# Optimization experiments

Measured on AMD Instinct MI355X. Metric: run time of the kernel, lower is better.

The kernel has to match this reference:

```python
import jax, jax.numpy as jnp
import numpy as np

EPS = 1e-5

def _bn(x):
    # training-mode batchnorm (batch stats), gamma=1 beta=0 per the module's init
    ax = tuple(range(x.ndim - 1))
    m = x.mean(ax, keepdims=True)
    v = x.var(ax, keepdims=True)
    return (x - m) * jax.lax.rsqrt(v + EPS)

def _mlp(x, weights):
    # shared 1x1-conv MLP: pointwise linear -> BN -> ReLU
    for W in weights:
        x = jax.nn.relu(_bn(jnp.einsum('...c,oc->...o', x, W)))
    return x

def _fps_single(xyz, npoint):
    # farthest point sampling, xyz [N,3] -> [npoint] int32 indices
    N = xyz.shape[0]
    def step(carry, _):
        dists, far = carry
        d = jnp.sum((xyz - xyz[far]) ** 2, -1)
        dists = jnp.minimum(dists, d)
        return (dists, jnp.argmax(dists).astype(jnp.int32)), far
    init = (jnp.full((N,), 1e10, xyz.dtype), jnp.int32(0))
    _, idx = jax.lax.scan(step, init, None, length=npoint)
    return idx

def _ball_query(new_xyz, xyz, radius, nsample):
    # first nsample points (in original order) within radius of each center
    d2 = jnp.sum((new_xyz[:, :, None, :] - xyz[:, None, :, :]) ** 2, -1)  # [B,S,N]
    N = xyz.shape[1]
    rank = jnp.where(d2 < radius * radius, jnp.arange(N, dtype=jnp.int32), jnp.int32(N))
    vals, _ = jax.lax.top_k(-rank, nsample)
    idx = -vals
    idx = jnp.where(idx == N, idx[..., :1], idx)  # pad with first valid (center itself)
    return idx

def _gather(pts, idx):
    # pts [B,N,C], idx [B,S,ns] -> [B,S,ns,C]
    B, S, ns = idx.shape
    return jnp.take_along_axis(pts, idx.reshape(B, S * ns, 1), axis=1).reshape(B, S, ns, pts.shape[-1])

def _sa(xyz, feats, npoint, radius, nsample, weights):
    fps_idx = jax.vmap(_fps_single, in_axes=(0, None))(xyz, npoint)
    new_xyz = jnp.take_along_axis(xyz, fps_idx[:, :, None], axis=1)  # [B,S,3]
    idx = _ball_query(new_xyz, xyz, radius, nsample)
    g_xyz = (_gather(xyz, idx) - new_xyz[:, :, None, :]) / radius  # normalize_xyz
    x = g_xyz if feats is None else jnp.concatenate([g_xyz, _gather(feats, idx)], -1)
    x = _mlp(x, weights)
    return new_xyz, x.max(axis=2), fps_idx  # maxpool over nsample

def _forward(obj_cloud, gripper_cloud, sa1_w0, sa1_w1, sa1_w2, sa2_w0, sa2_w1, sa2_w2,
             sa3_w0, sa3_w1, sa3_w2, ge_w0, ge_w1, ge_w2,
             head_w0, head_b0, head_w1, head_b1, head_w2, head_b2):
    # gripper encoder: pointwise conv1d MLP + global maxpool
    g = _mlp(gripper_cloud, [ge_w0, ge_w1, ge_w2])      # [B,G,128]
    gripper_feature = g.max(axis=1)                      # [B,128]
    # backbone
    xyz1, f1, _ = _sa(obj_cloud, None, 512, 0.2, 32, [sa1_w0, sa1_w1, sa1_w2])
    xyz2, f2, _ = _sa(xyz1, f1, 128, 0.4, 64, [sa2_w0, sa2_w1, sa2_w2])
    # sa3: group_all (use_xyz, no centering/normalization)
    x = jnp.concatenate([xyz2, f2], -1)[:, None]         # [B,1,128,259]
    x = _mlp(x, [sa3_w0, sa3_w1, sa3_w2])
    obj_feature = x.max(axis=2)[:, 0]                    # [B,1024]
    comb = jnp.concatenate([gripper_feature, obj_feature], -1)  # [B,1152]
    h = _bn(comb)
    h = jax.nn.relu(_bn(h @ head_w0.T + head_b0))
    h = jax.nn.relu(_bn(h @ head_w1.T + head_b1))
    return jax.nn.relu(h @ head_w2.T + head_b2)          # [B,1]

def setup_inputs() -> dict:
    key = jax.random.key(0)
    ks = jax.random.split(key, 24)
    def w(k, o, i):
        return (jax.random.normal(k, (o, i), jnp.float32) * 0.05)
    inp = {
        'obj_cloud': jax.random.uniform(ks[0], (8, 20000, 3), jnp.float32),
        'gripper_cloud': jax.random.uniform(ks[1], (8, 512, 3), jnp.float32),
        'sa1_w0': w(ks[2], 64, 3),   'sa1_w1': w(ks[3], 64, 64),   'sa1_w2': w(ks[4], 128, 64),
        'sa2_w0': w(ks[5], 128, 131),'sa2_w1': w(ks[6], 128, 128), 'sa2_w2': w(ks[7], 256, 128),
        'sa3_w0': w(ks[8], 256, 259),'sa3_w1': w(ks[9], 512, 256), 'sa3_w2': w(ks[10], 1024, 512),
        'ge_w0': w(ks[11], 64, 3),   'ge_w1': w(ks[12], 128, 64),  'ge_w2': w(ks[13], 128, 128),
        'head_w0': w(ks[14], 512, 1152), 'head_b0': jnp.zeros((512,), jnp.float32),
        'head_w1': w(ks[15], 256, 512),  'head_b1': jnp.zeros((256,), jnp.float32),
        'head_w2': w(ks[16], 1, 256),    'head_b2': jnp.zeros((1,), jnp.float32),
    }
    return inp

def reference(obj_cloud, gripper_cloud, sa1_w0, sa1_w1, sa1_w2, sa2_w0, sa2_w1, sa2_w2,
              sa3_w0, sa3_w1, sa3_w2, ge_w0, ge_w1, ge_w2,
              head_w0, head_b0, head_w1, head_b1, head_w2, head_b2):
    return _forward(obj_cloud, gripper_cloud, sa1_w0, sa1_w1, sa1_w2, sa2_w0, sa2_w1, sa2_w2,
                    sa3_w0, sa3_w1, sa3_w2, ge_w0, ge_w1, ge_w2,
                    head_w0, head_b0, head_w1, head_b1, head_w2, head_b2)
```

## Files before the change

### kernel.cpp

```cpp
#include <hip/hip_runtime.h>
#include <cstddef>
#include <cstdint>

#define EPS_BN 1e-5f
#define NBINS 4
#define NEG_INF (-__builtin_inff())

template <bool FUSE_IN, bool FUSE_MAX>
__global__ __launch_bounds__(256) void gemm_xwt(const float* __restrict__ X,
                                                const float* __restrict__ Wm,
                                                float* __restrict__ Y,
                                                int R, int Cin, int Cout,
                                                const float* __restrict__ st_in, int Rin,
                                                float* __restrict__ st_out,
                                                float* __restrict__ pooled, int ns) {
  __shared__ __align__(16) float Xs[16][132];
  __shared__ __align__(16) float Ws[16][132];
  __shared__ float sMean[512], sScale[512];
  const int t  = threadIdx.x;
  const int r0 = blockIdx.x << 7;
  const int n0 = blockIdx.y << 7;
  const int tx = t & 15;
  const int ty = t >> 4;

  if constexpr (FUSE_IN) {
    const float inv = 1.f / (float)Rin;
    for (int k = t; k < Cin; k += 256) {
      float s = 0.f, q = 0.f;
#pragma unroll
      for (int bn = 0; bn < NBINS; ++bn) {
        s += st_in[bn * 2 * Cin + k];
        q += st_in[bn * 2 * Cin + Cin + k];
      }
      const float m  = s * inv;
      const float vr = fmaf(-m, m, q * inv);
      sMean[k]  = m;
      sScale[k] = rsqrtf(vr + EPS_BN);
    }
    __syncthreads();
  }

  float acc[8][8] = {};
  const int rStage = t >> 1;
  const int kBase  = (t & 1) << 3;
  const int nr     = n0 + rStage;

  for (int k0 = 0; k0 < Cin; k0 += 16) {
    const float* xrow = X  + (size_t)(r0 + rStage) * Cin + k0 + kBase;
    const float* wrow = Wm + (size_t)nr * Cin + k0 + kBase;
    if (((Cin & 3) == 0) && (k0 + 16 <= Cin)) {
      float4 xa = *(const float4*)(xrow);
      float4 xb = *(const float4*)(xrow + 4);
      if constexpr (FUSE_IN) {
        const int kb = k0 + kBase;
        xa.x = fmaxf(0.f, (xa.x - sMean[kb + 0]) * sScale[kb + 0]);
        xa.y = fmaxf(0.f, (xa.y - sMean[kb + 1]) * sScale[kb + 1]);
        xa.z = fmaxf(0.f, (xa.z - sMean[kb + 2]) * sScale[kb + 2]);
        xa.w = fmaxf(0.f, (xa.w - sMean[kb + 3]) * sScale[kb + 3]);
        xb.x = fmaxf(0.f, (xb.x - sMean[kb + 4]) * sScale[kb + 4]);
        xb.y = fmaxf(0.f, (xb.y - sMean[kb + 5]) * sScale[kb + 5]);
        xb.z = fmaxf(0.f, (xb.z - sMean[kb + 6]) * sScale[kb + 6]);
        xb.w = fmaxf(0.f, (xb.w - sMean[kb + 7]) * sScale[kb + 7]);
      }
      Xs[kBase + 0][rStage] = xa.x; Xs[kBase + 1][rStage] = xa.y;
      Xs[kBase + 2][rStage] = xa.z; Xs[kBase + 3][rStage] = xa.w;
      Xs[kBase + 4][rStage] = xb.x; Xs[kBase + 5][rStage] = xb.y;
      Xs[kBase + 6][rStage] = xb.z; Xs[kBase + 7][rStage] = xb.w;
      float4 wa = {0, 0, 0, 0}, wb = {0, 0, 0, 0};
      if (nr < Cout) { wa = *(const float4*)(wrow); wb = *(const float4*)(wrow + 4); }
      Ws[kBase + 0][rStage] = wa.x; Ws[kBase + 1][rStage] = wa.y;
      Ws[kBase + 2][rStage] = wa.z; Ws[kBase + 3][rStage] = wa.w;
      Ws[kBase + 4][rStage] = wb.x; Ws[kBase + 5][rStage] = wb.y;
      Ws[kBase + 6][rStage] = wb.z; Ws[kBase + 7][rStage] = wb.w;
    } else {
#pragma unroll
      for (int u = 0; u < 8; ++u) {
        const int k = k0 + kBase + u;
        float xe = 0.f, we = 0.f;
        if (k < Cin) {
          xe = xrow[u];
          if constexpr (FUSE_IN) xe = fmaxf(0.f, (xe - sMean[k]) * sScale[k]);
          if (nr < Cout) we = wrow[u];
        }
        Xs[kBase + u][rStage] = xe;
        Ws[kBase + u][rStage] = we;
      }
    }
    __syncthreads();
#pragma unroll
    for (int kk = 0; kk < 16; ++kk) {
      const float4 a0 = *(const float4*)(&Xs[kk][ty << 2]);
      const float4 a1 = *(const float4*)(&Xs[kk][64 + (ty << 2)]);
      const float4 b0 = *(const float4*)(&Ws[kk][tx << 2]);
      const float4 b1 = *(const float4*)(&Ws[kk][64 + (tx << 2)]);
      const float av[8] = {a0.x, a0.y, a0.z, a0.w, a1.x, a1.y, a1.z, a1.w};
      const float bw[8] = {b0.x, b0.y, b0.z, b0.w, b1.x, b1.y, b1.z, b1.w};
#pragma unroll
      for (int i = 0; i < 8; ++i)
#pragma unroll
        for (int j = 0; j < 8; ++j) acc[i][j] = fmaf(av[i], bw[j], acc[i][j]);
    }
    __syncthreads();
  }
  if constexpr (!FUSE_MAX) {
#pragma unroll
    for (int h = 0; h < 2; ++h)
#pragma unroll
      for (int i = 0; i < 4; ++i) {
        const int r = r0 + h * 64 + (ty << 2) + i;
        float* yr = Y + (size_t)r * Cout;
#pragma unroll
        for (int g = 0; g < 2; ++g) {
          const int n = n0 + g * 64 + (tx << 2);
          if (n < Cout) {
            float4 o = {acc[h * 4 + i][g * 4 + 0], acc[h * 4 + i][g * 4 + 1],
                        acc[h * 4 + i][g * 4 + 2], acc[h * 4 + i][g * 4 + 3]};
            *(float4*)(yr + n) = o;
          }
        }
      }
  }
#pragma unroll
  for (int g = 0; g < 2; ++g)
#pragma unroll
    for (int j = 0; j < 4; ++j) {
      float s = 0.f, q = 0.f;
#pragma unroll
      for (int rh = 0; rh < 8; ++rh) {
        const float v = acc[rh][g * 4 + j];
        s += v;
        q = fmaf(v, v, q);
      }
      Xs[ty][g * 64 + (tx << 2) + j] = s;
      Ws[ty][g * 64 + (tx << 2) + j] = q;
    }
  __syncthreads();
  if (t < 128) {
    const int n = n0 + t;
    if (n < Cout) {
      float s = 0.f, q = 0.f;
#pragma unroll
      for (int w = 0; w < 16; ++w) { s += Xs[w][t]; q += Ws[w][t]; }
      float* dst = st_out + (blockIdx.x & (NBINS - 1)) * 2 * Cout;
      atomicAdd(dst + n, s);
      atomicAdd(dst + Cout + n, q);
    }
  }
  if constexpr (FUSE_MAX) {
    __syncthreads();
    float mxAll = NEG_INF;
#pragma unroll
    for (int h = 0; h < 2; ++h) {
#pragma unroll
      for (int g2 = 0; g2 < 2; ++g2)
#pragma unroll
        for (int j = 0; j < 4; ++j) {
          float mx = acc[h * 4 + 0][g2 * 4 + j];
          mx = fmaxf(mx, acc[h * 4 + 1][g2 * 4 + j]);
          mx = fmaxf(mx, acc[h * 4 + 2][g2 * 4 + j]);
          mx = fmaxf(mx, acc[h * 4 + 3][g2 * 4 + j]);
          Xs[ty][g2 * 64 + (tx << 2) + j] = mx;
        }
      __syncthreads();
      if (t < 128) {
        const int n = n0 + t;
        if (n < Cout) {
          if (ns <= 64) {
            const int tpg = ns >> 2;
            const int gph = 64 / ns;
            for (int gq = 0; gq < gph; ++gq) {
              float mx = NEG_INF;
              for (int w = gq * tpg; w < gq * tpg + tpg; ++w) mx = fmaxf(mx, Xs[w][t]);
              const int g = (r0 + h * 64) / ns + gq;
              pooled[(size_t)g * Cout + n] = mx;
            }
          } else {
            float mx = NEG_INF;
            for (int w = 0; w < 16; ++w) mx = fmaxf(mx, Xs[w][t]);
            mxAll = fmaxf(mxAll, mx);
          }
        }
      }
      __syncthreads();
    }
    if (ns > 64 && t < 128) {
      const int n = n0 + t;
      if (n < Cout) pooled[(size_t)(r0 >> 7) * Cout + n] = mxAll;
    }
  }
}

__global__ void bn_apply_pooled(const float* __restrict__ P, const float* __restrict__ st,
                                float* __restrict__ o, int G, int C, int Rtrue) {
  const int i = blockIdx.x * 256 + threadIdx.x;
  if (i >= G * C) return;
  const int c = i % C;
  float s = 0.f, q = 0.f;
#pragma unroll
  for (int bn = 0; bn < NBINS; ++bn) {
    s += st[bn * 2 * C + c];
    q += st[bn * 2 * C + C + c];
  }
  const float inv = 1.f / (float)Rtrue;
  const float m  = s * inv;
  const float vr = fmaf(-m, m, q * inv);
  const float sc = rsqrtf(vr + EPS_BN);
  o[i] = fmaxf(0.f, (P[i] - m) * sc);
}

__global__ void bn_apply_relu_maxpool(const float* __restrict__ Y,
                                      const float* __restrict__ st,
                                      float* __restrict__ o, int G, int ns, int C) {
  const int i = blockIdx.x * 256 + threadIdx.x;
  if (i >= G * C) return;
  const int c = i % C;
  const int g = i / C;
  float s = 0.f, q = 0.f;
#pragma unroll
  for (int bn = 0; bn < NBINS; ++bn) {
    s += st[bn * 2 * C + c];
    q += st[bn * 2 * C + C + c];
  }
  const int R = G * ns;
  const float inv = 1.f / (float)R;
  const float m  = s * inv;
  const float vr = fmaf(-m, m, q * inv);
  const float sc = rsqrtf(vr + EPS_BN);
  const float* p = Y + (size_t)g * ns * C + c;
  float mx = NEG_INF;
  for (int k = 0; k < ns; ++k) mx = fmaxf(mx, p[(size_t)k * C]);
  o[i] = fmaxf(0.f, (mx - m) * sc);
}

#define REPA(X) X(0) X(1) X(2) X(3) X(4) X(5) X(6) X(7) X(8) X(9) X(10) X(11)
#define REPB(X) X(12) X(13) X(14) X(15) X(16) X(17) X(18) X(19)

__global__ __launch_bounds__(1024)
void fps_sa1_kernel(const float* __restrict__ xyz, float* __restrict__ new_xyz) {
  const int b    = blockIdx.x;
  const int tid  = threadIdx.x;
  const int lane = tid & 63;
  const int wave = tid >> 6;
  const float* p = xyz + (size_t)b * 20000 * 3;

  __shared__ float ddL[12 * 1024];
  __shared__ float sv[16], sx[16], sy[16], sz[16];
  __shared__ int   si[16];
  __shared__ float bc[3];

#define DECLR(k) float px##k, py##k, pz##k, dd##k;
  REPB(DECLR)
#undef DECLR

#define INITL(k) ddL[(k) * 1024 + tid] = 1e10f;
  REPA(INITL)
#undef INITL
#define INITR(k) {                                                          \
    const int i = tid + (k) * 1024;                                         \
    if (i < 20000) {                                                        \
      px##k = p[i * 3 + 0]; py##k = p[i * 3 + 1]; pz##k = p[i * 3 + 2];     \
      dd##k = 1e10f;                                                        \
    } else {                                                                \
      px##k = 0.f; py##k = 0.f; pz##k = 0.f;                                \
      dd##k = NEG_INF;                                                      \
    } }
  REPB(INITR)
#undef INITR

  float fx = p[0], fy = p[1], fz = p[2];
  if (tid == 0) {
    float* o = new_xyz + (size_t)b * 512 * 3;
    o[0] = fx; o[1] = fy; o[2] = fz;
  }
  __syncthreads();

  for (int s = 1; s < 512; ++s) {
    float bv = NEG_INF;
    int   bi = 0x7fffffff;
    float bx = 0.f, by = 0.f, bz = 0.f;
#define SCANS(k) {                                                          \
    const int i = tid + (k) * 1024;                                         \
    const float qx = p[i * 3 + 0], qy = p[i * 3 + 1], qz = p[i * 3 + 2];    \
    const float dx = qx - fx, dy = qy - fy, dz = qz - fz;                   \
    const float d  = __fadd_rn(__fadd_rn(__fmul_rn(dx, dx), __fmul_rn(dy, dy)), \
                               __fmul_rn(dz, dz));                          \
    const float nd = fminf(ddL[(k) * 1024 + tid], d);                       \
    ddL[(k) * 1024 + tid] = nd;                                             \
    if (nd > bv) { bv = nd; bi = i; bx = qx; by = qy; bz = qz; } }
    REPA(SCANS)
#undef SCANS
#define SCANR(k) {                                                          \
    const float dx = px##k - fx, dy = py##k - fy, dz = pz##k - fz;          \
    const float d  = __fadd_rn(__fadd_rn(__fmul_rn(dx, dx), __fmul_rn(dy, dy)), \
                               __fmul_rn(dz, dz));                          \
    const float nd = fminf(dd##k, d);                                       \
    dd##k = nd;                                                             \
    if (nd > bv) { bv = nd; bi = tid + (k) * 1024;                          \
                   bx = px##k; by = py##k; bz = pz##k; } }
    REPB(SCANR)
#undef SCANR
    float v  = bv;
    int   i0 = bi;
#pragma unroll
    for (int m = 1; m < 64; m <<= 1) {
      const float ov = __shfl_xor(v, m, 64);
      const int   oi = __shfl_xor(i0, m, 64);
      if (ov > v || (ov == v && oi < i0)) { v = ov; i0 = oi; }
    }
    if (i0 == bi) {
      sv[wave] = bv; si[wave] = bi; sx[wave] = bx; sy[wave] = by; sz[wave] = bz;
    }
    __syncthreads();
    if (tid < 64) {
      const float lv = (lane < 16) ? sv[lane] : NEG_INF;
      const int   li = (lane < 16) ? si[lane] : 0x7fffffff;
      float v2 = lv;
      int   i2 = li;
#pragma unroll
      for (int m = 1; m < 16; m <<= 1) {
        const float ov = __shfl_xor(v2, m, 64);
        const int   oi = __shfl_xor(i2, m, 64);
        if (ov > v2 || (ov == v2 && oi < i2)) { v2 = ov; i2 = oi; }
      }
      if (lane < 16 && li == i2) {
        const float wx = sx[lane], wy = sy[lane], wz = sz[lane];
        bc[0] = wx; bc[1] = wy; bc[2] = wz;
        float* o = new_xyz + ((size_t)b * 512 + s) * 3;
        o[0] = wx; o[1] = wy; o[2] = wz;
      }
    }
    __syncthreads();
    fx = bc[0]; fy = bc[1]; fz = bc[2];
  }
}

template <int N, int NP, int THREADS, int NPT>
__global__ __launch_bounds__(THREADS)
void fps2_kernel(const float* __restrict__ xyz, float* __restrict__ new_xyz) {
  constexpr int NW = THREADS / 64;
  const int b    = blockIdx.x;
  const int tid  = threadIdx.x;
  const int lane = tid & 63;
  const int wave = tid >> 6;
  const float* p = xyz + (size_t)b * N * 3;
  float px[NPT], py[NPT], pz[NPT], dd[NPT];
#pragma unroll
  for (int j = 0; j < NPT; ++j) {
    const int i = tid + j * THREADS;
    if (i < N) {
      px[j] = p[i * 3 + 0];
      py[j] = p[i * 3 + 1];
      pz[j] = p[i * 3 + 2];
      dd[j] = 1e10f;
    } else {
      px[j] = 0.f; py[j] = 0.f; pz[j] = 0.f;
      dd[j] = NEG_INF;
    }
  }
  __shared__ float sv[NW], sx[NW], sy[NW], sz[NW];
  __shared__ int   si[NW];
  __shared__ float bc[3];
  float fx = p[0], fy = p[1], fz = p[2];
  if (tid == 0) {
    float* o = new_xyz + (size_t)b * NP * 3;
    o[0] = fx; o[1] = fy; o[2] = fz;
  }
  for (int s = 1; s < NP; ++s) {
    float bv = NEG_INF;
    int   bi = 0x7fffffff;
    float bx = 0.f, by = 0.f, bz = 0.f;
#pragma unroll
    for (int j = 0; j < NPT; ++j) {
      const float dx = px[j] - fx;
      const float dy = py[j] - fy;
      const float dz = pz[j] - fz;
      const float d  = __fadd_rn(__fadd_rn(__fmul_rn(dx, dx), __fmul_rn(dy, dy)),
                                 __fmul_rn(dz, dz));
      const float nd = fminf(dd[j], d);
      dd[j] = nd;
      if (nd > bv) { bv = nd; bi = tid + j * THREADS; bx = px[j]; by = py[j]; bz = pz[j]; }
    }
    float v = bv;
    int   i0 = bi;
#pragma unroll
    for (int m = 1; m < 64; m <<= 1) {
      const float ov = __shfl_xor(v, m, 64);
      const int   oi = __shfl_xor(i0, m, 64);
      if (ov > v || (ov == v && oi < i0)) { v = ov; i0 = oi; }
    }
    if (i0 == bi) {
      sv[wave] = bv; si[wave] = bi; sx[wave] = bx; sy[wave] = by; sz[wave] = bz;
    }
    __syncthreads();
    if (tid < 64) {
      const float lv = (lane < NW) ? sv[lane] : NEG_INF;
      const int   li = (lane < NW) ? si[lane] : 0x7fffffff;
      float v2 = lv;
      int   i2 = li;
#pragma unroll
      for (int m = 1; m < NW; m <<= 1) {
        const float ov = __shfl_xor(v2, m, 64);
        const int   oi = __shfl_xor(i2, m, 64);
        if (ov > v2 || (ov == v2 && oi < i2)) { v2 = ov; i2 = oi; }
      }
      if (lane < NW && li == i2) {
        const float wx = sx[lane], wy = sy[lane], wz = sz[lane];
        bc[0] = wx; bc[1] = wy; bc[2] = wz;
        float* o = new_xyz + ((size_t)b * NP + s) * 3;
        o[0] = wx; o[1] = wy; o[2] = wz;
      }
    }
    __syncthreads();
    fx = bc[0]; fy = bc[1]; fz = bc[2];
  }
}

template <int N, int NS>
__global__ __launch_bounds__(256)
void ballquery_wave_kernel(const float* __restrict__ centers,
                           const float* __restrict__ pts,
                           int* __restrict__ idx, int BS, int S, float r2) {
  const int w    = (blockIdx.x * 256 + threadIdx.x) >> 6;
  const int lane = threadIdx.x & 63;
  if (w >= BS) return;
  const int b = w / S;
  const float cx = centers[w * 3 + 0];
  const float cy = centers[w * 3 + 1];
  const float cz = centers[w * 3 + 2];
  const float* p = pts + (size_t)b * N * 3;
  int* o = idx + (size_t)w * NS;
  int total = 0;
  int first = -1;
  for (int i0 = 0; i0 < N && total < NS; i0 += 64) {
    const int i = i0 + lane;
    bool pred = false;
    if (i < N) {
      const float dx = cx - p[i * 3 + 0];
      const float dy = cy - p[i * 3 + 1];
      const float dz = cz - p[i * 3 + 2];
      const float d2 = __fadd_rn(__fadd_rn(__fmul_rn(dx, dx), __fmul_rn(dy, dy)),
                                 __fmul_rn(dz, dz));
      pred = (d2 < r2);
    }
    const unsigned long long mask = __ballot(pred);
    if (mask) {
      const unsigned long long below = (lane == 0) ? 0ull : (mask << (64 - lane));
      const int before = __popcll(below);
      if (pred && (total + before) < NS) o[total + before] = i;
      if (first < 0) first = i0 + (__ffsll((long long)mask) - 1);
      total += __popcll(mask);
    }
  }
  if (lane >= total && lane < NS) o[lane] = first;
}

__global__ void group1_kernel(const float* __restrict__ xyz, const float* __restrict__ ctr,
                              const int* __restrict__ idx, float* __restrict__ X1) {
  const int t = blockIdx.x * 256 + threadIdx.x;
  if (t >= 8 * 512 * 32) return;
  const int g = t >> 5;
  const int b = g >> 9;
  const int i = idx[t];
  const float* p = xyz + ((size_t)b * 20000 + i) * 3;
  const float* c = ctr + (size_t)g * 3;
  X1[t * 3 + 0] = (p[0] - c[0]) / 0.2f;
  X1[t * 3 + 1] = (p[1] - c[1]) / 0.2f;
  X1[t * 3 + 2] = (p[2] - c[2]) / 0.2f;
}

__global__ void group2_kernel(const float* __restrict__ xyz1,
                              const float* __restrict__ xyz2,
                              const float* __restrict__ f1,
                              const int* __restrict__ idx2,
                              float* __restrict__ X2) {
  const int t = blockIdx.x * 256 + threadIdx.x;
  if (t >= 65536 * 131) return;
  const int r = t / 131;
  const int c = t - r * 131;
  const int g = r >> 6;
  const int b = g >> 7;
  const int i = idx2[r];
  float v;
  if (c < 3) {
    v = (xyz1[((size_t)b * 512 + i) * 3 + c] - xyz2[(size_t)g * 3 + c]) / 0.4f;
  } else {
    v = f1[((size_t)b * 512 + i) * 128 + (c - 3)];
  }
  X2[t] = v;
}

__global__ void build_x3_kernel(const float* __restrict__ xyz2, const float* __restrict__ f2,
                                float* __restrict__ X3) {
  const int t = blockIdx.x * 256 + threadIdx.x;
  if (t >= 1024 * 259) return;
  const int r = t / 259;
  const int c = t - r * 259;
  X3[t] = (c < 3) ? xyz2[r * 3 + c] : f2[(size_t)r * 256 + (c - 3)];
}

__global__ __launch_bounds__(512) void head_kernel(
    const float* __restrict__ gfeat, const float* __restrict__ objf,
    const float* __restrict__ w0, const float* __restrict__ b0,
    const float* __restrict__ w1, const float* __restrict__ b1,
    const float* __restrict__ w2, const float* __restrict__ b2,
    float* __restrict__ out) {
  __shared__ __align__(16) float comb[8 * 1152];
  __shared__ __align__(16) float h1[8 * 512];
  __shared__ __align__(16) float h2[8 * 256];
  const int tid = threadIdx.x;
  for (int i = tid; i < 8 * 1152; i += 512) {
    const int b = i / 1152, c = i - b * 1152;
    comb[i] = (c < 128) ? gfeat[b * 128 + c] : objf[b * 1024 + (c - 128)];
  }
  __syncthreads();
  for (int c = tid; c < 1152; c += 512) {
    float s = 0.f;
#pragma unroll
    for (int b = 0; b < 8; ++b) s += comb[b * 1152 + c];
    const float m = s * 0.125f;
    float v = 0.f;
#pragma unroll
    for (int b = 0; b < 8; ++b) { const float d = comb[b * 1152 + c] - m; v = fmaf(d, d, v); }
    const float sc = rsqrtf(v * 0.125f + EPS_BN);
#pragma unroll
    for (int b = 0; b < 8; ++b) comb[b * 1152 + c] = (comb[b * 1152 + c] - m) * sc;
  }
  __syncthreads();
  {
    float a[8];
#pragma unroll
    for (int b = 0; b < 8; ++b) a[b] = b0[tid];
    const float* wr = w0 + (size_t)tid * 1152;
    for (int ci = 0; ci < 1152; ci += 4) {
      const float4 wv = *(const float4*)(wr + ci);
#pragma unroll
      for (int b = 0; b < 8; ++b) {
        const float4 xv = *(const float4*)(&comb[b * 1152 + ci]);
        a[b] = fmaf(xv.x, wv.x, a[b]);
        a[b] = fmaf(xv.y, wv.y, a[b]);
        a[b] = fmaf(xv.z, wv.z, a[b]);
        a[b] = fmaf(xv.w, wv.w, a[b]);
      }
    }
    float s = 0.f;
#pragma unroll
    for (int b = 0; b < 8; ++b) s += a[b];
    const float m = s * 0.125f;
    float v = 0.f;
#pragma unroll
    for (int b = 0; b < 8; ++b) { const float d = a[b] - m; v = fmaf(d, d, v); }
    const float sc = rsqrtf(v * 0.125f + EPS_BN);
#pragma unroll
    for (int b = 0; b < 8; ++b) h1[b * 512 + tid] = fmaxf(0.f, (a[b] - m) * sc);
  }
  __syncthreads();
  if (tid < 256) {
    float a[8];
#pragma unroll
    for (int b = 0; b < 8; ++b) a[b] = b1[tid];
    const float* wr = w1 + (size_t)tid * 512;
    for (int ci = 0; ci < 512; ci += 4) {
      const float4 wv = *(const float4*)(wr + ci);
#pragma unroll
      for (int b = 0; b < 8; ++b) {
        const float4 xv = *(const float4*)(&h1[b * 512 + ci]);
        a[b] = fmaf(xv.x, wv.x, a[b]);
        a[b] = fmaf(xv.y, wv.y, a[b]);
        a[b] = fmaf(xv.z, wv.z, a[b]);
        a[b] = fmaf(xv.w, wv.w, a[b]);
      }
    }
    float s = 0.f;
#pragma unroll
    for (int b = 0; b < 8; ++b) s += a[b];
    const float m = s * 0.125f;
    float v = 0.f;
#pragma unroll
    for (int b = 0; b < 8; ++b) { const float d = a[b] - m; v = fmaf(d, d, v); }
    const float sc = rsqrtf(v * 0.125f + EPS_BN);
#pragma unroll
    for (int b = 0; b < 8; ++b) h2[b * 256 + tid] = fmaxf(0.f, (a[b] - m) * sc);
  }
  __syncthreads();
  if (tid < 8) {
    float s = b2[0];
    for (int ci = 0; ci < 256; ++ci) s = fmaf(h2[tid * 256 + ci], w2[ci], s);
    out[tid] = fmaxf(0.f, s);
  }
}

extern "C" void kernel_launch(void* const* d_in, const int* in_sizes, int n_in,
                              void* d_out, int out_size, void* d_ws, size_t ws_size,
                              hipStream_t stream) {
  (void)in_sizes; (void)n_in; (void)out_size; (void)ws_size;
  const float* obj  = (const float*)d_in[0];
  const float* grip = (const float*)d_in[1];
  const float* s1w0 = (const float*)d_in[2];
  const float* s1w1 = (const float*)d_in[3];
  const float* s1w2 = (const float*)d_in[4];
  const float* s2w0 = (const float*)d_in[5];
  const float* s2w1 = (const float*)d_in[6];
  const float* s2w2 = (const float*)d_in[7];
  const float* s3w0 = (const float*)d_in[8];
  const float* s3w1 = (const float*)d_in[9];
  const float* s3w2 = (const float*)d_in[10];
  const float* gw0  = (const float*)d_in[11];
  const float* gw1  = (const float*)d_in[12];
  const float* gw2  = (const float*)d_in[13];
  const float* hw0  = (const float*)d_in[14];
  const float* hb0  = (const float*)d_in[15];
  const float* hw1  = (const float*)d_in[16];
  const float* hb1  = (const float*)d_in[17];
  const float* hw2  = (const float*)d_in[18];
  const float* hb2  = (const float*)d_in[19];
  float* out = (float*)d_out;

  float* wsf   = (float*)d_ws;
  float* stats = wsf;
  float* xyz1  = wsf + 23040;
  float* xyz2  = wsf + 35328;
  float* gfeat = wsf + 38400;
  float* objf  = wsf + 39424;
  float* f1    = wsf + 47616;
  float* f2    = wsf + 571904;
  float* x3    = wsf + 834048;
  int*   idx1  = (int*)(wsf + 1099264);
  int*   idx2  = (int*)(wsf + 1230336);
  float* bufP  = wsf + 1295872;
  float* bufQ  = wsf + 18073088;

  static const int st_off[12] = {0, 512, 1536, 2560, 3072, 3584,
                                 4608, 5632, 6656, 8704, 10752, 14848};
  auto st = [&](int li) { return stats + st_off[li]; };

  hipMemsetAsync(stats, 0, 23040 * sizeof(float), stream);

  auto gemm0 = [&](const float* X, const float* Wm, float* Y, int R, int Cin, int Cout,
                   int lo) {
    dim3 g((R + 127) / 128, (Cout + 127) / 128);
    gemm_xwt<false, false><<<g, 256, 0, stream>>>(X, Wm, Y, R, Cin, Cout, nullptr, 0,
                                                  st(lo), nullptr, 0);
  };
  auto gemmf = [&](const float* X, const float* Wm, float* Y, int R, int Cin, int Cout,
                   int li, int lo) {
    dim3 g((R + 127) / 128, (Cout + 127) / 128);
    gemm_xwt<true, false><<<g, 256, 0, stream>>>(X, Wm, Y, R, Cin, Cout, st(li), R,
                                                 st(lo), nullptr, 0);
  };
  auto gemmfM = [&](const float* X, const float* Wm, float* pooled, int R, int Cin,
                    int Cout, int li, int lo, int ns) {
    dim3 g((R + 127) / 128, (Cout + 127) / 128);
    gemm_xwt<true, true><<<g, 256, 0, stream>>>(X, Wm, nullptr, R, Cin, Cout, st(li), R,
                                                st(lo), pooled, ns);
  };
  auto applymax_k = [&](const float* Y, int li, int G, int ns, int C, float* o) {
    const int n = G * C;
    bn_apply_relu_maxpool<<<(n + 255) / 256, 256, 0, stream>>>(Y, st(li), o, G, ns, C);
  };
  auto applypool_k = [&](const float* P, int li, int G, int C, int Rtrue, float* o) {
    const int n = G * C;
    bn_apply_pooled<<<(n + 255) / 256, 256, 0, stream>>>(P, st(li), o, G, C, Rtrue);
  };

  fps_sa1_kernel<<<8, 1024, 0, stream>>>(obj, xyz1);

  float* gY1 = bufP;
  float* gY2 = bufP + 262144;
  float* gY3 = bufP + 786432;
  gemm0(grip, gw0, gY1, 4096, 3, 64, 0);
  gemmf(gY1, gw1, gY2, 4096, 64, 128, 0, 1);
  gemmf(gY2, gw2, gY3, 4096, 128, 128, 1, 2);
  applymax_k(gY3, 2, 8, 512, 128, gfeat);

  ballquery_wave_kernel<20000, 32><<<1024, 256, 0, stream>>>(xyz1, obj, idx1, 4096, 512, 0.04f);
  float* X1 = bufQ;
  group1_kernel<<<512, 256, 0, stream>>>(obj, xyz1, idx1, X1);
  gemm0(X1, s1w0, bufP, 131072, 3, 64, 3);
  gemmf(bufP, s1w1, bufQ, 131072, 64, 64, 3, 4);
  gemmfM(bufQ, s1w2, bufP, 131072, 64, 128, 4, 5, 32);
  applypool_k(bufP, 5, 4096, 128, 131072, f1);

  fps2_kernel<512, 128, 256, 2><<<8, 256, 0, stream>>>(xyz1, xyz2);
  ballquery_wave_kernel<512, 64><<<256, 256, 0, stream>>>(xyz2, xyz1, idx2, 1024, 128, 0.16f);
  float* X2 = bufQ;
  group2_kernel<<<(65536 * 131 + 255) / 256, 256, 0, stream>>>(xyz1, xyz2, f1, idx2, X2);
  gemm0(X2, s2w0, bufP, 65536, 131, 128, 6);
  gemmf(bufP, s2w1, bufQ, 65536, 128, 128, 6, 7);
  gemmfM(bufQ, s2w2, bufP, 65536, 128, 256, 7, 8, 64);
  applypool_k(bufP, 8, 1024, 256, 65536, f2);

  build_x3_kernel<<<(1024 * 259 + 255) / 256, 256, 0, stream>>>(xyz2, f2, x3);
  float* Y3a = bufQ;
  float* Y3b = bufQ + 262144;
  float* Y3p = bufQ + 786432;
  gemm0(x3, s3w0, Y3a, 1024, 259, 256, 9);
  gemmf(Y3a, s3w1, Y3b, 1024, 256, 512, 9, 10);
  gemmfM(Y3b, s3w2, Y3p, 1024, 512, 1024, 10, 11, 128);
  applypool_k(Y3p, 11, 8, 1024, 1024, objf);

  head_kernel<<<1, 512, 0, stream>>>(gfeat, objf, hw0, hb0, hw1, hb1, hw2, hb2, out);
}
```

Measured before the change: 2.432 ms.

## Accelerate SA1 farthest point sampling with spatial grid cell pruning

Replaces the brute-force FPS scan over all 20000 points with a 6x6x6 uniform grid. Points are bucketed by cell and their per-point min distances kept in LDS. Each iteration only rescans cells whose lower-bound distance to the new center could shrink the cell's cached max, then reduces over per-cell maxima. This cuts the per-step distance work, at the cost of setup passes, global scratch storage, serialized per-wave cell loops and load imbalance across waves.

```diff
diff --git a/kernel.cpp b/kernel.cpp
--- a/kernel.cpp
+++ b/kernel.cpp
@@ -232,100 +232,187 @@
   o[i] = fmaxf(0.f, (mx - m) * sc);
 }
 
-#define REPA(X) X(0) X(1) X(2) X(3) X(4) X(5) X(6) X(7) X(8) X(9) X(10) X(11)
-#define REPB(X) X(12) X(13) X(14) X(15) X(16) X(17) X(18) X(19)
+#define FPS_N 20000
+#define FPS_S 512
+#define FPS_NC 6
+#define FPS_NCELL 216
 
 __global__ __launch_bounds__(1024)
-void fps_sa1_kernel(const float* __restrict__ xyz, float* __restrict__ new_xyz) {
+void fps_sa1_kernel(const float* __restrict__ xyz, float* __restrict__ new_xyz,
+                    float* __restrict__ scratch) {
   const int b    = blockIdx.x;
   const int tid  = threadIdx.x;
   const int lane = tid & 63;
   const int wave = tid >> 6;
-  const float* p = xyz + (size_t)b * 20000 * 3;
-
-  __shared__ float ddL[12 * 1024];
-  __shared__ float sv[16], sx[16], sy[16], sz[16];
-  __shared__ int   si[16];
+  const float* p = xyz + (size_t)b * FPS_N * 3;
+  float* gxs = scratch + (size_t)b * FPS_N * 4;
+  float* gys = gxs + FPS_N;
+  float* gzs = gys + FPS_N;
+  int*   gis = (int*)(gzs + FPS_N);
+
+  __shared__ float ddS[FPS_N];
+  __shared__ int   cStart[FPS_NCELL + 1];
+  __shared__ int   cCnt[FPS_NCELL];
+  __shared__ int   cFill[FPS_NCELL];
+  __shared__ float ubV[FPS_NCELL];
+  __shared__ int   ubI[FPS_NCELL];
+  __shared__ float ubX[FPS_NCELL], ubY[FPS_NCELL], ubZ[FPS_NCELL];
   __shared__ float bc[3];
-
-#define DECLR(k) float px##k, py##k, pz##k, dd##k;
-  REPB(DECLR)
-#undef DECLR
-
-#define INITL(k) ddL[(k) * 1024 + tid] = 1e10f;
-  REPA(INITL)
-#undef INITL
-#define INITR(k) {                                                          \
-    const int i = tid + (k) * 1024;                                         \
-    if (i < 20000) {                                                        \
-      px##k = p[i * 3 + 0]; py##k = p[i * 3 + 1]; pz##k = p[i * 3 + 2];     \
-      dd##k = 1e10f;                                                        \
-    } else {                                                                \
-      px##k = 0.f; py##k = 0.f; pz##k = 0.f;                                \
-      dd##k = NEG_INF;                                                      \
-    } }
-  REPB(INITR)
-#undef INITR
+  __shared__ float wred[16 * 6];
+  __shared__ float sC[10];
+
+  float mnx = 1e30f, mny = 1e30f, mnz = 1e30f;
+  float mxx = -1e30f, mxy = -1e30f, mxz = -1e30f;
+  for (int i = tid; i < FPS_N; i += 1024) {
+    const float x = p[i * 3 + 0], y = p[i * 3 + 1], z = p[i * 3 + 2];
+    mnx = fminf(mnx, x); mny = fminf(mny, y); mnz = fminf(mnz, z);
+    mxx = fmaxf(mxx, x); mxy = fmaxf(mxy, y); mxz = fmaxf(mxz, z);
+  }
+#pragma unroll
+  for (int m = 1; m < 64; m <<= 1) {
+    mnx = fminf(mnx, __shfl_xor(mnx, m, 64));
+    mny = fminf(mny, __shfl_xor(mny, m, 64));
+    mnz = fminf(mnz, __shfl_xor(mnz, m, 64));
+    mxx = fmaxf(mxx, __shfl_xor(mxx, m, 64));
+    mxy = fmaxf(mxy, __shfl_xor(mxy, m, 64));
+    mxz = fmaxf(mxz, __shfl_xor(mxz, m, 64));
+  }
+  if (lane == 0) {
+    wred[wave * 6 + 0] = mnx; wred[wave * 6 + 1] = mny; wred[wave * 6 + 2] = mnz;
+    wred[wave * 6 + 3] = mxx; wred[wave * 6 + 4] = mxy; wred[wave * 6 + 5] = mxz;
+  }
+  if (tid < FPS_NCELL) { cCnt[tid] = 0; cFill[tid] = 0; }
+  __syncthreads();
+  if (tid == 0) {
+    float a0 = wred[0], a1 = wred[1], a2 = wred[2];
+    float a3 = wred[3], a4 = wred[4], a5 = wred[5];
+    for (int w = 1; w < 16; ++w) {
+      a0 = fminf(a0, wred[w * 6 + 0]); a1 = fminf(a1, wred[w * 6 + 1]);
+      a2 = fminf(a2, wred[w * 6 + 2]); a3 = fmaxf(a3, wred[w * 6 + 3]);
+      a4 = fmaxf(a4, wred[w * 6 + 4]); a5 = fmaxf(a5, wred[w * 6 + 5]);
+    }
+    const float ex = fmaxf(a3 - a0, 1e-9f);
+    const float ey = fmaxf(a4 - a1, 1e-9f);
+    const float ez = fmaxf(a5 - a2, 1e-9f);
+    sC[0] = a0; sC[1] = a1; sC[2] = a2;
+    sC[3] = (float)FPS_NC / ex; sC[4] = (float)FPS_NC / ey; sC[5] = (float)FPS_NC / ez;
+    sC[6] = ex / (float)FPS_NC; sC[7] = ey / (float)FPS_NC; sC[8] = ez / (float)FPS_NC;
+    sC[9] = fmaxf(ex, fmaxf(ey, ez)) * 1e-5f;
+  }
+  __syncthreads();
+  const float bx0 = sC[0], by0 = sC[1], bz0 = sC[2];
+  const float scx = sC[3], scy = sC[4], scz = sC[5];
+  const float hx  = sC[6], hy  = sC[7], hz  = sC[8], ec = sC[9];
+
+  for (int i = tid; i < FPS_N; i += 1024) {
+    const float x = p[i * 3 + 0], y = p[i * 3 + 1], z = p[i * 3 + 2];
+    const int cx = min(FPS_NC - 1, max(0, (int)((x - bx0) * scx)));
+    const int cy = min(FPS_NC - 1, max(0, (int)((y - by0) * scy)));
+    const int cz = min(FPS_NC - 1, max(0, (int)((z - bz0) * scz)));
+    atomicAdd(&cCnt[(cx * FPS_NC + cy) * FPS_NC + cz], 1);
+  }
+  __syncthreads();
+  if (tid == 0) {
+    int acc = 0;
+    for (int k = 0; k < FPS_NCELL; ++k) { cStart[k] = acc; acc += cCnt[k]; }
+    cStart[FPS_NCELL] = acc;
+  }
+  __syncthreads();
+  for (int i = tid; i < FPS_N; i += 1024) {
+    const float x = p[i * 3 + 0], y = p[i * 3 + 1], z = p[i * 3 + 2];
+    const int cx = min(FPS_NC - 1, max(0, (int)((x - bx0) * scx)));
+    const int cy = min(FPS_NC - 1, max(0, (int)((y - by0) * scy)));
+    const int cz = min(FPS_NC - 1, max(0, (int)((z - bz0) * scz)));
+    const int cid = (cx * FPS_NC + cy) * FPS_NC + cz;
+    const int pos = cStart[cid] + atomicAdd(&cFill[cid], 1);
+    gxs[pos] = x; gys[pos] = y; gzs[pos] = z; gis[pos] = i;
+  }
+  for (int j = tid; j < FPS_N; j += 1024) ddS[j] = 1e10f;
+  if (tid < FPS_NCELL) {
+    ubV[tid] = (cCnt[tid] > 0) ? 1e10f : NEG_INF;
+    ubI[tid] = 0x7fffffff;
+  }
+  __syncthreads();
 
   float fx = p[0], fy = p[1], fz = p[2];
   if (tid == 0) {
-    float* o = new_xyz + (size_t)b * 512 * 3;
+    float* o = new_xyz + (size_t)b * FPS_S * 3;
     o[0] = fx; o[1] = fy; o[2] = fz;
   }
-  __syncthreads();
-
-  for (int s = 1; s < 512; ++s) {
-    float bv = NEG_INF;
-    int   bi = 0x7fffffff;
-    float bx = 0.f, by = 0.f, bz = 0.f;
-#define SCANS(k) {                                                          \
-    const int i = tid + (k) * 1024;                                         \
-    const float qx = p[i * 3 + 0], qy = p[i * 3 + 1], qz = p[i * 3 + 2];    \
-    const float dx = qx - fx, dy = qy - fy, dz = qz - fz;                   \
-    const float d  = __fadd_rn(__fadd_rn(__fmul_rn(dx, dx), __fmul_rn(dy, dy)), \
-                               __fmul_rn(dz, dz));                          \
-    const float nd = fminf(ddL[(k) * 1024 + tid], d);                       \
-    ddL[(k) * 1024 + tid] = nd;                                             \
-    if (nd > bv) { bv = nd; bi = i; bx = qx; by = qy; bz = qz; } }
-    REPA(SCANS)
-#undef SCANS
-#define SCANR(k) {                                                          \
-    const float dx = px##k - fx, dy = py##k - fy, dz = pz##k - fz;          \
-    const float d  = __fadd_rn(__fadd_rn(__fmul_rn(dx, dx), __fmul_rn(dy, dy)), \
-                               __fmul_rn(dz, dz));                          \
-    const float nd = fminf(dd##k, d);                                       \
-    dd##k = nd;                                                             \
-    if (nd > bv) { bv = nd; bi = tid + (k) * 1024;                          \
-                   bx = px##k; by = py##k; bz = pz##k; } }
-    REPB(SCANR)
-#undef SCANR
-    float v  = bv;
-    int   i0 = bi;
-#pragma unroll
-    for (int m = 1; m < 64; m <<= 1) {
-      const float ov = __shfl_xor(v, m, 64);
-      const int   oi = __shfl_xor(i0, m, 64);
-      if (ov > v || (ov == v && oi < i0)) { v = ov; i0 = oi; }
-    }
-    if (i0 == bi) {
-      sv[wave] = bv; si[wave] = bi; sx[wave] = bx; sy[wave] = by; sz[wave] = bz;
+
+  for (int s = 1; s < FPS_S; ++s) {
+    const int cq = wave + (lane << 4);
+    bool aff = false;
+    if (cq < FPS_NCELL) {
+      const int cx  = cq / (FPS_NC * FPS_NC);
+      const int rem = cq - cx * (FPS_NC * FPS_NC);
+      const int cy  = rem / FPS_NC;
+      const int cz  = rem - cy * FPS_NC;
+      const float lox = fmaf((float)cx, hx, bx0) - ec;
+      const float hix = fmaf((float)(cx + 1), hx, bx0) + ec;
+      const float loy = fmaf((float)cy, hy, by0) - ec;
+      const float hiy = fmaf((float)(cy + 1), hy, by0) + ec;
+      const float loz = fmaf((float)cz, hz, bz0) - ec;
+      const float hiz = fmaf((float)(cz + 1), hz, bz0) + ec;
+      const float dx = fmaxf(0.f, fmaxf(lox - fx, fx - hix));
+      const float dy = fmaxf(0.f, fmaxf(loy - fy, fy - hiy));
+      const float dz = fmaxf(0.f, fmaxf(loz - fz, fz - hiz));
+      const float dmin = dx * dx + dy * dy + dz * dz;
+      aff = (dmin * 0.99999f < ubV[cq]);
+    }
+    unsigned long long am = __ballot(aff);
+    while (am) {
+      const int l = __ffsll((long long)am) - 1;
+      am &= am - 1;
+      const int cc  = wave + (l << 4);
+      const int st0 = cStart[cc];
+      const int cn  = cStart[cc + 1] - st0;
+      float bv = NEG_INF; int bi = 0x7fffffff;
+      float bx = 0.f, by = 0.f, bz = 0.f;
+      for (int j = lane; j < cn; j += 64) {
+        const int g = st0 + j;
+        const float qx = gxs[g], qy = gys[g], qz = gzs[g];
+        const float dx = qx - fx, dy = qy - fy, dz = qz - fz;
+        const float d  = __fadd_rn(__fadd_rn(__fmul_rn(dx, dx), __fmul_rn(dy, dy)),
+                                   __fmul_rn(dz, dz));
+        const float nd = fminf(ddS[g], d);
+        ddS[g] = nd;
+        const int gi = gis[g];
+        if (nd > bv || (nd == bv && gi < bi)) { bv = nd; bi = gi; bx = qx; by = qy; bz = qz; }
+      }
+      float v = bv; int i0 = bi;
+#pragma unroll
+      for (int m = 1; m < 64; m <<= 1) {
+        const float ov = __shfl_xor(v, m, 64);
+        const int   oi = __shfl_xor(i0, m, 64);
+        if (ov > v || (ov == v && oi < i0)) { v = ov; i0 = oi; }
+      }
+      if (v == bv && i0 == bi && bi != 0x7fffffff) {
+        ubV[cc] = v; ubI[cc] = i0; ubX[cc] = bx; ubY[cc] = by; ubZ[cc] = bz;
+      }
     }
     __syncthreads();
     if (tid < 64) {
-      const float lv = (lane < 16) ? sv[lane] : NEG_INF;
-      const int   li = (lane < 16) ? si[lane] : 0x7fffffff;
-      float v2 = lv;
-      int   i2 = li;
-#pragma unroll
-      for (int m = 1; m < 16; m <<= 1) {
-        const float ov = __shfl_xor(v2, m, 64);
-        const int   oi = __shfl_xor(i2, m, 64);
-        if (ov > v2 || (ov == v2 && oi < i2)) { v2 = ov; i2 = oi; }
-      }
-      if (lane < 16 && li == i2) {
-        const float wx = sx[lane], wy = sy[lane], wz = sz[lane];
+      float v = NEG_INF; int i0 = 0x7fffffff; int c0 = 0;
+#pragma unroll
+      for (int q = 0; q < 4; ++q) {
+        const int k = lane + (q << 6);
+        if (k < FPS_NCELL) {
+          const float ov = ubV[k]; const int oi = ubI[k];
+          if (ov > v || (ov == v && oi < i0)) { v = ov; i0 = oi; c0 = k; }
+        }
+      }
+#pragma unroll
+      for (int m = 1; m < 64; m <<= 1) {
+        const float ov = __shfl_xor(v, m, 64);
+        const int   oi = __shfl_xor(i0, m, 64);
+        const int   oc = __shfl_xor(c0, m, 64);
+        if (ov > v || (ov == v && oi < i0)) { v = ov; i0 = oi; c0 = oc; }
+      }
+      if (lane == 0) {
+        const float wx = ubX[c0], wy = ubY[c0], wz = ubZ[c0];
         bc[0] = wx; bc[1] = wy; bc[2] = wz;
-        float* o = new_xyz + ((size_t)b * 512 + s) * 3;
+        float* o = new_xyz + ((size_t)b * FPS_S + s) * 3;
         o[0] = wx; o[1] = wy; o[2] = wz;
       }
     }
@@ -628,6 +715,7 @@
   int*   idx2  = (int*)(wsf + 1230336);
   float* bufP  = wsf + 1295872;
   float* bufQ  = wsf + 18073088;
+  float* fpsScratch = bufP + 8388608;
 
   static const int st_off[12] = {0, 512, 1536, 2560, 3072, 3584,
                                  4608, 5632, 6656, 8704, 10752, 14848};
@@ -662,7 +750,7 @@
     bn_apply_pooled<<<(n + 255) / 256, 256, 0, stream>>>(P, st(li), o, G, C, Rtrue);
   };
 
-  fps_sa1_kernel<<<8, 1024, 0, stream>>>(obj, xyz1);
+  fps_sa1_kernel<<<8, 1024, 0, stream>>>(obj, xyz1, fpsScratch);
 
   float* gY1 = bufP;
   float* gY2 = bufP + 262144;
```

New measurement: 2.662 ms. 9.5% more time.
